# Performance work log

Hardware: AMD Instinct MI355X
Metric: run time of the kernel (lower is better)

The kernel has to match this reference:

```python
import jax, jax.numpy as jnp
import numpy as np

NUM_EMB = 1024
EMB_DIM = 256
COMM_COST = 0.25
BETA = 0.25


def setup_inputs() -> dict:
    key = jax.random.key(0)
    k1, k2 = jax.random.split(key)
    x = jax.random.normal(k1, (16, EMB_DIM, 64, 64), dtype=jnp.float32)
    # nn.Embedding initialized uniform(-1/num_emb, 1/num_emb)
    emb_weight = jax.random.uniform(
        k2, (NUM_EMB, EMB_DIM), dtype=jnp.float32,
        minval=-1.0 / NUM_EMB, maxval=1.0 / NUM_EMB)
    return {"x": x, "emb_weight": emb_weight}


def reference(x, emb_weight):
    # x: [B, C, H, W] -> [B, H, W, C]
    xp = jnp.transpose(x, (0, 2, 3, 1))
    B, H, W, C = xp.shape
    flat = xp.reshape(-1, C)  # [N, C]
    # squared euclidean distances (argmin-equivalent to torch.cdist)
    d2 = (jnp.sum(flat * flat, axis=1, keepdims=True)
          - 2.0 * jnp.einsum('nc,kc->nk', flat, emb_weight)
          + jnp.sum(emb_weight * emb_weight, axis=1))  # [N, K]
    idx = jnp.argmin(d2, axis=1)  # [N]
    quantized = emb_weight[idx].reshape(B, H, W, C)
    e_latent_loss = jnp.mean((jax.lax.stop_gradient(quantized) - xp) ** 2) * BETA
    q_latent_loss = jnp.mean((quantized - jax.lax.stop_gradient(xp)) ** 2)
    c_loss = q_latent_loss + COMM_COST * e_latent_loss
    # straight-through estimator
    quant_st = xp + jax.lax.stop_gradient(quantized - xp)
    quant_out = jnp.transpose(quant_st, (0, 3, 1, 2))  # [B, C, H, W]
    return (c_loss, quant_out)
```

## Files before the change

kernel.cpp:

```cpp
#include <hip/hip_runtime.h>
#include <hip/hip_bf16.h>
#include <cstdint>
#include <cstddef>

#define EMB_K   1024
#define EMB_C   256
#define HWB     4096
#define NPIX    65536

typedef __bf16 bf16x8 __attribute__((ext_vector_type(8)));
typedef float  f32x4  __attribute__((ext_vector_type(4)));

__device__ __forceinline__ unsigned short bf16bits(float v) {
  __hip_bfloat16 h = __float2bfloat16(v);
  return __builtin_bit_cast(unsigned short, h);
}

__global__ void k_emb(const float* __restrict__ emb, unsigned short* __restrict__ emb_bf,
                      float* __restrict__ enorm, float* __restrict__ loss,
                      unsigned* __restrict__ ctr) {
  int k = blockIdx.x;
  int c = threadIdx.x;
  if (k == 0 && c == 0) { *loss = 0.f; *ctr = 0u; }
  float v = emb[(size_t)k * EMB_C + c];
  emb_bf[(size_t)k * EMB_C + c] = bf16bits(v);
  float s = v * v;
  for (int m = 32; m; m >>= 1) s += __shfl_down(s, m, 64);
  __shared__ float red[4];
  int lane = c & 63, w = c >> 6;
  if (lane == 0) red[w] = s;
  __syncthreads();
  if (c == 0) enorm[k] = red[0] + red[1] + red[2] + red[3];
}

__device__ __forceinline__ void stage_b64(const unsigned short* __restrict__ embbf,
                                          unsigned char* buf, int kt, int t) {
#pragma unroll
  for (int j = 0; j < 4; ++j) {
    int d = j * 512 + t;
    int r = d >> 5;
    int slot = d & 31;
    int c16 = ((slot >> 3) << 3) | ((slot & 7) ^ (r & 7));
    const unsigned short* src = embbf + (size_t)(kt * 64 + r) * EMB_C + c16 * 8;
    __builtin_amdgcn_global_load_lds(
        (const __attribute__((address_space(1))) void*)src,
        (__attribute__((address_space(3))) void*)(buf + (unsigned)(j * 8192 + (t >> 6) * 1024)),
        16, 0, 0);
  }
}

#define LDS_BYTES 70688

__global__ __launch_bounds__(512, 4) void
k_main(const float* __restrict__ x, const float* __restrict__ emb,
       const unsigned short* __restrict__ embbf, const float* __restrict__ enorm,
       float* __restrict__ out, float* __restrict__ loss, unsigned* __restrict__ ctr) {
  extern __shared__ char smem[];
  unsigned char* R0 = (unsigned char*)smem;
  unsigned char* R1 = (unsigned char*)(smem + 32768);
  float*    cjl    = (float*)(smem + 65536);
  unsigned* keys_l = (unsigned*)(smem + 69632);
  float*    xn_l   = (float*)(smem + 70144);
  float*    red    = (float*)(smem + 70656);

  int n0  = blockIdx.x * 128;
  int b   = n0 >> 12;
  int hw0 = n0 & 4095;
  int t    = threadIdx.x;
  int w    = t >> 6, lane = t & 63;
  int quad = lane >> 4, lr = lane & 15;
  int g = w >> 1;
  int h = w & 1;

  for (int i = t; i < 1024; i += 512) cjl[i] = 0.375f - 0.5f * enorm[i];
  if (t < 128) { keys_l[t] = 0u; xn_l[t] = 0.f; }
  __syncthreads();

  {
    int nl = (w & 1) * 64 + lane;
    const float* xp = x + (size_t)b * (EMB_C * HWB) + hw0 + nl;
    float xn = 0.f;
#pragma unroll
    for (int o = 0; o < 8; ++o) {
      int cc = (w >> 1) * 8 + o;
      float v[8];
#pragma unroll
      for (int j = 0; j < 8; ++j) {
        v[j] = xp[(size_t)(cc * 8 + j) * HWB];
        xn += v[j] * v[j];
      }
      union { unsigned u[4]; uint4 q; } pk;
#pragma unroll
      for (int m = 0; m < 4; ++m)
        pk.u[m] = (unsigned)bf16bits(v[2 * m]) | ((unsigned)bf16bits(v[2 * m + 1]) << 16);
      int pos = ((cc >> 3) << 3) | ((cc & 7) ^ (nl & 7));
      *(uint4*)(R0 + nl * 512 + pos * 16) = pk.q;
    }
    atomicAdd(&xn_l[nl], xn);
  }
  __syncthreads();

  bf16x8 af[2][8];
#pragma unroll
  for (int i = 0; i < 2; ++i) {
    int rA = g * 32 + i * 16 + lr;
#pragma unroll
    for (int s = 0; s < 8; ++s) {
      int cc = s * 4 + quad;
      int pos = ((cc >> 3) << 3) | ((cc & 7) ^ (rA & 7));
      af[i][s] = *(const bf16x8*)(R0 + rA * 512 + pos * 16);
    }
  }
  __syncthreads();

  stage_b64(embbf, R0, 0, t);
  __syncthreads();

  unsigned best[2][4] = {{0u,0u,0u,0u},{0u,0u,0u,0u}};
  for (int kt = 0; kt < 16; ++kt) {
    unsigned char* srcB = (kt & 1) ? R1 : R0;
    unsigned char* dstB = (kt & 1) ? R0 : R1;
    if (kt < 15) stage_b64(embbf, dstB, kt + 1, t);
    float cj[2]; unsigned kp[2];
#pragma unroll
    for (int j = 0; j < 2; ++j) {
      int k = kt * 64 + h * 32 + j * 16 + lr;
      cj[j] = cjl[k];
      kp[j] = 1023u - (unsigned)k;
    }
    f32x4 acc[2][2] = {};
#pragma unroll
    for (int s = 0; s < 8; ++s) {
      bf16x8 bf[2];
#pragma unroll
      for (int j = 0; j < 2; ++j) {
        int rB = h * 32 + j * 16 + lr;
        int cc = s * 4 + quad;
        int pos = ((cc >> 3) << 3) | ((cc & 7) ^ (rB & 7));
        bf[j] = *(const bf16x8*)(srcB + rB * 512 + pos * 16);
      }
#pragma unroll
      for (int i = 0; i < 2; ++i)
#pragma unroll
        for (int j = 0; j < 2; ++j)
          acc[i][j] = __builtin_amdgcn_mfma_f32_16x16x32_bf16(af[i][s], bf[j], acc[i][j], 0, 0, 0);
    }
#pragma unroll
    for (int i = 0; i < 2; ++i)
#pragma unroll
      for (int j = 0; j < 2; ++j)
#pragma unroll
        for (int r = 0; r < 4; ++r) {
          float f = acc[i][j][r] + cj[j];
          unsigned key = (__float_as_uint(f) & 0xFFFFFC00u) | kp[j];
          best[i][r] = best[i][r] > key ? best[i][r] : key;
        }
    __syncthreads();
  }

#pragma unroll
  for (int i = 0; i < 2; ++i)
#pragma unroll
    for (int r = 0; r < 4; ++r) {
      unsigned v = best[i][r];
#pragma unroll
      for (int m = 1; m < 16; m <<= 1) {
        unsigned o = (unsigned)__shfl_xor((int)v, m, 64);
        v = v > o ? v : o;
      }
      if (lr == 0) atomicMax(&keys_l[g * 32 + i * 16 + quad * 4 + r], v);
    }
  __syncthreads();

  if (t < 128) {
    unsigned key = keys_l[t];
    float fh = __uint_as_float(key & 0xFFFFFC00u);
    float lsum = xn_l[t] + 0.75f - 2.0f * fh;
    for (int m = 32; m; m >>= 1) lsum += __shfl_down(lsum, m, 64);
    if (lane == 0) red[w] = lsum;
  }
  __syncthreads();
  if (t == 0) {
    atomicAdd(loss, red[0] + red[1]);
    __threadfence();
  }

  float* tile = (float*)R0;
  int nl  = t & 127;
  int cs  = (t >> 7) * 32;
  int idx = 1023 - (int)(keys_l[nl] & 1023u);
  float* ob = out + 1 + (size_t)b * (EMB_C * HWB) + hw0;
  for (int hc = 0; hc < 2; ++hc) {
    if (hc) __syncthreads();
    const float* er = emb + (size_t)idx * EMB_C + hc * 128 + cs;
#pragma unroll
    for (int m = 0; m < 8; ++m) {
      f32x4 q = *(const f32x4*)(er + m * 4);
      tile[(cs + m * 4 + 0) * 128 + nl] = q[0];
      tile[(cs + m * 4 + 1) * 128 + nl] = q[1];
      tile[(cs + m * 4 + 2) * 128 + nl] = q[2];
      tile[(cs + m * 4 + 3) * 128 + nl] = q[3];
    }
    __syncthreads();
#pragma unroll
    for (int s2 = 0; s2 < 32; ++s2) {
      int id = s2 * 512 + t;
      int cl = id >> 7;
      int nn = id & 127;
      ob[(size_t)(hc * 128 + cl) * HWB + nn] = tile[cl * 128 + nn];
    }
  }

  if (t == 0) {
    unsigned done = atomicAdd(ctr, 1u);
    if (done == gridDim.x - 1) {
      float total = atomicAdd(loss, 0.f);
      out[0] = 1.0625f * total / 16777216.0f;
    }
  }
}

extern "C" void kernel_launch(void* const* d_in, const int* in_sizes, int n_in,
                              void* d_out, int out_size, void* d_ws, size_t ws_size,
                              hipStream_t stream) {
  const float* x   = (const float*)d_in[0];
  const float* emb = (const float*)d_in[1];
  float* out = (float*)d_out;
  char*  ws  = (char*)d_ws;

  unsigned short* emb_bf = (unsigned short*)ws;
  float*          enorm  = (float*)(ws + 524288);
  float*          loss   = (float*)(ws + 528384);
  unsigned*       ctr    = (unsigned*)(ws + 528388);

  hipFuncSetAttribute((const void*)k_main,
                      hipFuncAttributeMaxDynamicSharedMemorySize, LDS_BYTES);

  k_emb <<<dim3(EMB_K), dim3(EMB_C), 0, stream>>>(emb, emb_bf, enorm, loss, ctr);
  k_main<<<dim3(NPIX / 128), dim3(512), LDS_BYTES, stream>>>(x, emb, emb_bf, enorm,
                                                             out, loss, ctr);
}
```

Measured before the change: 177.8 us.

## Split fused VQ kernel into transpose, GEMM-argmin, and gather-output kernels

Breaks the single fused kernel into three. The first transposes x and converts it to bf16 into a scratch area inside the output buffer, also producing per-pixel norms. The second is a GEMM with argmin whose warps now cover 64 rows by 16 codes each, with launch bounds lowered to 2 blocks. The third gathers codebook rows and writes the transposed output with vectorised stores. The aim is to separate memory-bound phases from the MFMA loop and make them more efficient, at the cost of extra launches and writing then re-reading the bf16 copy of x through global memory.

```diff
diff --git a/kernel.cpp b/kernel.cpp
--- a/kernel.cpp
+++ b/kernel.cpp
@@ -10,6 +10,7 @@
 
 typedef __bf16 bf16x8 __attribute__((ext_vector_type(8)));
 typedef float  f32x4  __attribute__((ext_vector_type(4)));
+typedef float  f32x4a __attribute__((ext_vector_type(4), aligned(4)));
 
 __device__ __forceinline__ unsigned short bf16bits(float v) {
   __hip_bfloat16 h = __float2bfloat16(v);
@@ -33,15 +34,57 @@
   if (c == 0) enorm[k] = red[0] + red[1] + red[2] + red[3];
 }
 
-__device__ __forceinline__ void stage_b64(const unsigned short* __restrict__ embbf,
-                                          unsigned char* buf, int kt, int t) {
+__global__ __launch_bounds__(256) void
+k_tr(const float* __restrict__ x, unsigned short* __restrict__ A,
+     float* __restrict__ xn_g) {
+  __shared__ unsigned char tile[64 * 512];
+  __shared__ float xn_l[64];
+  int t  = threadIdx.x;
+  int n0 = blockIdx.x * 64;
+  int b  = n0 >> 12, hw0 = n0 & 4095;
+  int nl = t & 63, qq = t >> 6;
+  if (t < 64) xn_l[t] = 0.f;
+  __syncthreads();
+  const float* xp = x + (size_t)b * (EMB_C * HWB) + hw0 + nl;
+  float xn = 0.f;
+#pragma unroll
+  for (int o = 0; o < 8; ++o) {
+    int cc = qq * 8 + o;
+    float v[8];
+#pragma unroll
+    for (int j = 0; j < 8; ++j) {
+      v[j] = xp[(size_t)(cc * 8 + j) * HWB];
+      xn += v[j] * v[j];
+    }
+    union { unsigned u[4]; uint4 q; } pk;
+#pragma unroll
+    for (int m = 0; m < 4; ++m)
+      pk.u[m] = (unsigned)bf16bits(v[2 * m]) | ((unsigned)bf16bits(v[2 * m + 1]) << 16);
+    int pos = ((cc >> 3) << 3) | ((cc & 7) ^ (nl & 7));
+    *(uint4*)(tile + nl * 512 + pos * 16) = pk.q;
+  }
+  atomicAdd(&xn_l[nl], xn);
+  __syncthreads();
+  if (t < 64) xn_g[n0 + t] = xn_l[t];
+  uint4* Adst = (uint4*)A + (size_t)n0 * 32;
+#pragma unroll
+  for (int k = 0; k < 8; ++k) {
+    int id = k * 256 + t;
+    int n = id >> 5, slot = id & 31;
+    int pos = ((slot >> 3) << 3) | ((slot & 7) ^ (n & 7));
+    Adst[id] = *(const uint4*)(tile + n * 512 + pos * 16);
+  }
+}
+
+__device__ __forceinline__ void stage64(const unsigned short* __restrict__ rows,
+                                        unsigned char* buf, int t) {
 #pragma unroll
   for (int j = 0; j < 4; ++j) {
     int d = j * 512 + t;
     int r = d >> 5;
     int slot = d & 31;
     int c16 = ((slot >> 3) << 3) | ((slot & 7) ^ (r & 7));
-    const unsigned short* src = embbf + (size_t)(kt * 64 + r) * EMB_C + c16 * 8;
+    const unsigned short* src = rows + (size_t)r * EMB_C + c16 * 8;
     __builtin_amdgcn_global_load_lds(
         (const __attribute__((address_space(1))) void*)src,
         (__attribute__((address_space(3))) void*)(buf + (unsigned)(j * 8192 + (t >> 6) * 1024)),
@@ -49,12 +92,13 @@
   }
 }
 
-#define LDS_BYTES 70688
-
-__global__ __launch_bounds__(512, 4) void
-k_main(const float* __restrict__ x, const float* __restrict__ emb,
-       const unsigned short* __restrict__ embbf, const float* __restrict__ enorm,
-       float* __restrict__ out, float* __restrict__ loss, unsigned* __restrict__ ctr) {
+#define K2_LDS 70688
+
+__global__ __launch_bounds__(512, 2) void
+k_gemm(const unsigned short* __restrict__ A, const unsigned short* __restrict__ embbf,
+       const float* __restrict__ enorm, const float* __restrict__ xn_g,
+       unsigned* __restrict__ keys_g, float* __restrict__ out,
+       float* __restrict__ loss, unsigned* __restrict__ ctr) {
   extern __shared__ char smem[];
   unsigned char* R0 = (unsigned char*)smem;
   unsigned char* R1 = (unsigned char*)(smem + 32768);
@@ -63,47 +107,22 @@
   float*    xn_l   = (float*)(smem + 70144);
   float*    red    = (float*)(smem + 70656);
 
-  int n0  = blockIdx.x * 128;
-  int b   = n0 >> 12;
-  int hw0 = n0 & 4095;
-  int t    = threadIdx.x;
-  int w    = t >> 6, lane = t & 63;
+  int n0 = blockIdx.x * 128;
+  int t = threadIdx.x, w = t >> 6, lane = t & 63;
   int quad = lane >> 4, lr = lane & 15;
-  int g = w >> 1;
-  int h = w & 1;
-
+  int g  = w >> 2;
+  int h2 = w & 3;
+
+  stage64(A + (size_t)n0 * EMB_C, R0, t);
+  stage64(A + (size_t)(n0 + 64) * EMB_C, R1, t);
   for (int i = t; i < 1024; i += 512) cjl[i] = 0.375f - 0.5f * enorm[i];
-  if (t < 128) { keys_l[t] = 0u; xn_l[t] = 0.f; }
-  __syncthreads();
-
-  {
-    int nl = (w & 1) * 64 + lane;
-    const float* xp = x + (size_t)b * (EMB_C * HWB) + hw0 + nl;
-    float xn = 0.f;
-#pragma unroll
-    for (int o = 0; o < 8; ++o) {
-      int cc = (w >> 1) * 8 + o;
-      float v[8];
-#pragma unroll
-      for (int j = 0; j < 8; ++j) {
-        v[j] = xp[(size_t)(cc * 8 + j) * HWB];
-        xn += v[j] * v[j];
-      }
-      union { unsigned u[4]; uint4 q; } pk;
-#pragma unroll
-      for (int m = 0; m < 4; ++m)
-        pk.u[m] = (unsigned)bf16bits(v[2 * m]) | ((unsigned)bf16bits(v[2 * m + 1]) << 16);
-      int pos = ((cc >> 3) << 3) | ((cc & 7) ^ (nl & 7));
-      *(uint4*)(R0 + nl * 512 + pos * 16) = pk.q;
-    }
-    atomicAdd(&xn_l[nl], xn);
-  }
-  __syncthreads();
-
-  bf16x8 af[2][8];
-#pragma unroll
-  for (int i = 0; i < 2; ++i) {
-    int rA = g * 32 + i * 16 + lr;
+  if (t < 128) { keys_l[t] = 0u; xn_l[t] = xn_g[n0 + t]; }
+  __syncthreads();
+
+  bf16x8 af[4][8];
+#pragma unroll
+  for (int i = 0; i < 4; ++i) {
+    int rA = g * 64 + i * 16 + lr;
 #pragma unroll
     for (int s = 0; s < 8; ++s) {
       int cc = s * 4 + quad;
@@ -113,53 +132,40 @@
   }
   __syncthreads();
 
-  stage_b64(embbf, R0, 0, t);
-  __syncthreads();
-
-  unsigned best[2][4] = {{0u,0u,0u,0u},{0u,0u,0u,0u}};
+  stage64(embbf, R0, t);
+  __syncthreads();
+
+  unsigned best[4][4] = {};
   for (int kt = 0; kt < 16; ++kt) {
     unsigned char* srcB = (kt & 1) ? R1 : R0;
     unsigned char* dstB = (kt & 1) ? R0 : R1;
-    if (kt < 15) stage_b64(embbf, dstB, kt + 1, t);
-    float cj[2]; unsigned kp[2];
-#pragma unroll
-    for (int j = 0; j < 2; ++j) {
-      int k = kt * 64 + h * 32 + j * 16 + lr;
-      cj[j] = cjl[k];
-      kp[j] = 1023u - (unsigned)k;
-    }
-    f32x4 acc[2][2] = {};
+    if (kt < 15) stage64(embbf + (size_t)(kt + 1) * 64 * EMB_C, dstB, t);
+    float cj; unsigned kp;
+    { int k = kt * 64 + h2 * 16 + lr; cj = cjl[k]; kp = 1023u - (unsigned)k; }
+    f32x4 acc[4] = {};
 #pragma unroll
     for (int s = 0; s < 8; ++s) {
-      bf16x8 bf[2];
-#pragma unroll
-      for (int j = 0; j < 2; ++j) {
-        int rB = h * 32 + j * 16 + lr;
-        int cc = s * 4 + quad;
-        int pos = ((cc >> 3) << 3) | ((cc & 7) ^ (rB & 7));
-        bf[j] = *(const bf16x8*)(srcB + rB * 512 + pos * 16);
+      int cc = s * 4 + quad;
+      int rB = h2 * 16 + lr;
+      int pos = ((cc >> 3) << 3) | ((cc & 7) ^ (rB & 7));
+      bf16x8 bf = *(const bf16x8*)(srcB + rB * 512 + pos * 16);
+#pragma unroll
+      for (int i = 0; i < 4; ++i)
+        acc[i] = __builtin_amdgcn_mfma_f32_16x16x32_bf16(af[i][s], bf, acc[i], 0, 0, 0);
+    }
+#pragma unroll
+    for (int i = 0; i < 4; ++i)
+#pragma unroll
+      for (int r = 0; r < 4; ++r) {
+        float f = acc[i][r] + cj;
+        unsigned key = (__float_as_uint(f) & 0xFFFFFC00u) | kp;
+        best[i][r] = best[i][r] > key ? best[i][r] : key;
       }
-#pragma unroll
-      for (int i = 0; i < 2; ++i)
-#pragma unroll
-        for (int j = 0; j < 2; ++j)
-          acc[i][j] = __builtin_amdgcn_mfma_f32_16x16x32_bf16(af[i][s], bf[j], acc[i][j], 0, 0, 0);
-    }
-#pragma unroll
-    for (int i = 0; i < 2; ++i)
-#pragma unroll
-      for (int j = 0; j < 2; ++j)
-#pragma unroll
-        for (int r = 0; r < 4; ++r) {
-          float f = acc[i][j][r] + cj[j];
-          unsigned key = (__float_as_uint(f) & 0xFFFFFC00u) | kp[j];
-          best[i][r] = best[i][r] > key ? best[i][r] : key;
-        }
     __syncthreads();
   }
 
 #pragma unroll
-  for (int i = 0; i < 2; ++i)
+  for (int i = 0; i < 4; ++i)
 #pragma unroll
     for (int r = 0; r < 4; ++r) {
       unsigned v = best[i][r];
@@ -168,12 +174,13 @@
         unsigned o = (unsigned)__shfl_xor((int)v, m, 64);
         v = v > o ? v : o;
       }
-      if (lr == 0) atomicMax(&keys_l[g * 32 + i * 16 + quad * 4 + r], v);
+      if (lr == 0) atomicMax(&keys_l[g * 64 + i * 16 + quad * 4 + r], v);
     }
   __syncthreads();
 
   if (t < 128) {
     unsigned key = keys_l[t];
+    keys_g[n0 + t] = key;
     float fh = __uint_as_float(key & 0xFFFFFC00u);
     float lsum = xn_l[t] + 0.75f - 2.0f * fh;
     for (int m = 32; m; m >>= 1) lsum += __shfl_down(lsum, m, 64);
@@ -183,39 +190,42 @@
   if (t == 0) {
     atomicAdd(loss, red[0] + red[1]);
     __threadfence();
-  }
-
-  float* tile = (float*)R0;
-  int nl  = t & 127;
-  int cs  = (t >> 7) * 32;
-  int idx = 1023 - (int)(keys_l[nl] & 1023u);
-  float* ob = out + 1 + (size_t)b * (EMB_C * HWB) + hw0;
-  for (int hc = 0; hc < 2; ++hc) {
-    if (hc) __syncthreads();
-    const float* er = emb + (size_t)idx * EMB_C + hc * 128 + cs;
-#pragma unroll
-    for (int m = 0; m < 8; ++m) {
-      f32x4 q = *(const f32x4*)(er + m * 4);
-      tile[(cs + m * 4 + 0) * 128 + nl] = q[0];
-      tile[(cs + m * 4 + 1) * 128 + nl] = q[1];
-      tile[(cs + m * 4 + 2) * 128 + nl] = q[2];
-      tile[(cs + m * 4 + 3) * 128 + nl] = q[3];
-    }
-    __syncthreads();
-#pragma unroll
-    for (int s2 = 0; s2 < 32; ++s2) {
-      int id = s2 * 512 + t;
-      int cl = id >> 7;
-      int nn = id & 127;
-      ob[(size_t)(hc * 128 + cl) * HWB + nn] = tile[cl * 128 + nn];
-    }
-  }
-
-  if (t == 0) {
     unsigned done = atomicAdd(ctr, 1u);
     if (done == gridDim.x - 1) {
       float total = atomicAdd(loss, 0.f);
       out[0] = 1.0625f * total / 16777216.0f;
+    }
+  }
+}
+
+__global__ __launch_bounds__(512) void
+k_out(const float* __restrict__ emb, const unsigned* __restrict__ keys_g,
+      float* __restrict__ out) {
+  extern __shared__ float tile[];
+  int t  = threadIdx.x;
+  int n0 = blockIdx.x * 256;
+  int b  = n0 >> 12, hw0 = n0 & 4095;
+  int w  = t >> 6, lane = t & 63;
+  int n  = t >> 1, ch = t & 1;
+  int idx = 1023 - (int)(keys_g[n0 + n] & 1023u);
+  const float* er = emb + (size_t)idx * EMB_C;
+  float* ob = out + 1 + (size_t)b * (EMB_C * HWB) + hw0;
+  for (int p = 0; p < 4; ++p) {
+    int c0 = p * 64;
+    if (p) __syncthreads();
+#pragma unroll
+    for (int jj = 0; jj < 8; ++jj) {
+      f32x4 q = *(const f32x4*)(er + c0 + ch * 32 + jj * 4);
+#pragma unroll
+      for (int m = 0; m < 4; ++m)
+        tile[(ch * 32 + jj * 4 + m) * 256 + n] = q[m];
+    }
+    __syncthreads();
+#pragma unroll
+    for (int cc = 0; cc < 8; ++cc) {
+      int cl = w * 8 + cc;
+      f32x4 q = *(const f32x4*)(tile + cl * 256 + lane * 4);
+      *(f32x4a*)(ob + (size_t)(c0 + cl) * HWB + lane * 4) = q;
     }
   }
 }
@@ -232,11 +242,19 @@
   float*          enorm  = (float*)(ws + 524288);
   float*          loss   = (float*)(ws + 528384);
   unsigned*       ctr    = (unsigned*)(ws + 528388);
-
-  hipFuncSetAttribute((const void*)k_main,
-                      hipFuncAttributeMaxDynamicSharedMemorySize, LDS_BYTES);
-
-  k_emb <<<dim3(EMB_K), dim3(EMB_C), 0, stream>>>(emb, emb_bf, enorm, loss, ctr);
-  k_main<<<dim3(NPIX / 128), dim3(512), LDS_BYTES, stream>>>(x, emb, emb_bf, enorm,
-                                                             out, loss, ctr);
-}
+  float*          xn_g   = (float*)(ws + 532480);
+  unsigned*       keys_g = (unsigned*)(ws + 794624);
+
+  unsigned short* A = (unsigned short*)(out + 4);
+
+  hipFuncSetAttribute((const void*)k_gemm,
+                      hipFuncAttributeMaxDynamicSharedMemorySize, K2_LDS);
+  hipFuncSetAttribute((const void*)k_out,
+                      hipFuncAttributeMaxDynamicSharedMemorySize, 65536);
+
+  k_emb <<<dim3(EMB_K),      dim3(EMB_C), 0,      stream>>>(emb, emb_bf, enorm, loss, ctr);
+  k_tr  <<<dim3(NPIX / 64),  dim3(256),   0,      stream>>>(x, A, xn_g);
+  k_gemm<<<dim3(NPIX / 128), dim3(512),   K2_LDS, stream>>>(A, emb_bf, enorm, xn_g,
+                                                            keys_g, out, loss, ctr);
+  k_out <<<dim3(NPIX / 256), dim3(512),   65536,  stream>>>(emb, keys_g, out);
+}
```

Result: slower. 187.1 us (+5.2%).

## Double pixel tile to 256 per 1024-thread block with vectorized x loads and stores

Applied to the files above, without the earlier changes.

Each block now covers 256 pixels with 1024 threads, so every staged 64-row codebook tile is reused by twice as many pixels and the total codebook traffic through LDS is halved. The x tile is loaded with float4 reads and packed to bf16 in two passes, and the output write uses a rotated LDS tile so that unaligned output (offset by one float for the loss slot) can be written with float4 stores. In exchange, blocks are larger with fewer resident per CU, and the grid is halved, which may reduce latency hiding and load balance.

```diff
diff --git a/kernel.cpp b/kernel.cpp
--- a/kernel.cpp
+++ b/kernel.cpp
@@ -33,118 +33,120 @@
   if (c == 0) enorm[k] = red[0] + red[1] + red[2] + red[3];
 }
 
-__device__ __forceinline__ void stage_b64(const unsigned short* __restrict__ embbf,
-                                          unsigned char* buf, int kt, int t) {
-#pragma unroll
-  for (int j = 0; j < 4; ++j) {
-    int d = j * 512 + t;
+__device__ __forceinline__ void stage64b(const unsigned short* __restrict__ rows,
+                                         unsigned char* buf, int t) {
+#pragma unroll
+  for (int j = 0; j < 2; ++j) {
+    int d = j * 1024 + t;
     int r = d >> 5;
     int slot = d & 31;
     int c16 = ((slot >> 3) << 3) | ((slot & 7) ^ (r & 7));
-    const unsigned short* src = embbf + (size_t)(kt * 64 + r) * EMB_C + c16 * 8;
+    const unsigned short* src = rows + (size_t)r * EMB_C + c16 * 8;
     __builtin_amdgcn_global_load_lds(
         (const __attribute__((address_space(1))) void*)src,
-        (__attribute__((address_space(3))) void*)(buf + (unsigned)(j * 8192 + (t >> 6) * 1024)),
+        (__attribute__((address_space(3))) void*)(buf + (unsigned)(j * 16384 + (t >> 6) * 1024)),
         16, 0, 0);
   }
 }
 
-#define LDS_BYTES 70688
-
-__global__ __launch_bounds__(512, 4) void
+#define LDS_BYTES 71744
+
+__global__ __launch_bounds__(1024) void
 k_main(const float* __restrict__ x, const float* __restrict__ emb,
        const unsigned short* __restrict__ embbf, const float* __restrict__ enorm,
        float* __restrict__ out, float* __restrict__ loss, unsigned* __restrict__ ctr) {
   extern __shared__ char smem[];
-  unsigned char* R0 = (unsigned char*)smem;
-  unsigned char* R1 = (unsigned char*)(smem + 32768);
   float*    cjl    = (float*)(smem + 65536);
   unsigned* keys_l = (unsigned*)(smem + 69632);
-  float*    xn_l   = (float*)(smem + 70144);
-  float*    red    = (float*)(smem + 70656);
-
-  int n0  = blockIdx.x * 128;
-  int b   = n0 >> 12;
-  int hw0 = n0 & 4095;
-  int t    = threadIdx.x;
-  int w    = t >> 6, lane = t & 63;
+  float*    xn_l   = (float*)(smem + 70656);
+  float*    red    = (float*)(smem + 71680);
+
+  int n0 = blockIdx.x * 256;
+  int b  = n0 >> 12, hw0 = n0 & 4095;
+  int t = threadIdx.x, w = t >> 6, lane = t & 63;
   int quad = lane >> 4, lr = lane & 15;
-  int g = w >> 1;
-  int h = w & 1;
-
-  for (int i = t; i < 1024; i += 512) cjl[i] = 0.375f - 0.5f * enorm[i];
-  if (t < 128) { keys_l[t] = 0u; xn_l[t] = 0.f; }
-  __syncthreads();
-
-  {
-    int nl = (w & 1) * 64 + lane;
-    const float* xp = x + (size_t)b * (EMB_C * HWB) + hw0 + nl;
-    float xn = 0.f;
-#pragma unroll
-    for (int o = 0; o < 8; ++o) {
-      int cc = (w >> 1) * 8 + o;
-      float v[8];
+  int g  = w >> 1;
+  int h2 = w & 1;
+
+  if (t < 256) { keys_l[t] = 0u; xn_l[t] = 0.f; }
+  for (int i = t; i < 1024; i += 1024) cjl[i] = 0.375f - 0.5f * enorm[i];
+  __syncthreads();
+
+  bf16x8 af[2][8];
+#pragma unroll
+  for (int p = 0; p < 2; ++p) {
+    if (p) __syncthreads();
+    {
+      int hwq = t & 31;
+      int cg  = t >> 5;
+      const float* xp = x + (size_t)b * (EMB_C * HWB) + hw0 + p * 128 + hwq * 4;
+      float xn[4] = {0.f, 0.f, 0.f, 0.f};
+      unsigned pk[4][4] = {};
 #pragma unroll
       for (int j = 0; j < 8; ++j) {
-        v[j] = xp[(size_t)(cc * 8 + j) * HWB];
-        xn += v[j] * v[j];
-      }
-      union { unsigned u[4]; uint4 q; } pk;
-#pragma unroll
-      for (int m = 0; m < 4; ++m)
-        pk.u[m] = (unsigned)bf16bits(v[2 * m]) | ((unsigned)bf16bits(v[2 * m + 1]) << 16);
-      int pos = ((cc >> 3) << 3) | ((cc & 7) ^ (nl & 7));
-      *(uint4*)(R0 + nl * 512 + pos * 16) = pk.q;
-    }
-    atomicAdd(&xn_l[nl], xn);
-  }
-  __syncthreads();
-
-  bf16x8 af[2][8];
-#pragma unroll
-  for (int i = 0; i < 2; ++i) {
-    int rA = g * 32 + i * 16 + lr;
+        f32x4 v = *(const f32x4*)(xp + (size_t)(cg * 8 + j) * HWB);
+#pragma unroll
+        for (int m = 0; m < 4; ++m) {
+          xn[m] += v[m] * v[m];
+          pk[m][j >> 1] |= (unsigned)bf16bits(v[m]) << ((j & 1) * 16);
+        }
+      }
+#pragma unroll
+      for (int m = 0; m < 4; ++m) {
+        int nl = hwq * 4 + m;
+        int pos = ((cg >> 3) << 3) | ((cg & 7) ^ (nl & 7));
+        *(uint4*)(smem + nl * 512 + pos * 16) = *(const uint4*)pk[m];
+        atomicAdd(&xn_l[p * 128 + nl], xn[m]);
+      }
+    }
+    __syncthreads();
+    if ((g >> 2) == p) {
+#pragma unroll
+      for (int i = 0; i < 2; ++i) {
+        int rA = (g & 3) * 32 + i * 16 + lr;
+#pragma unroll
+        for (int s = 0; s < 8; ++s) {
+          int cc = s * 4 + quad;
+          int pos = ((cc >> 3) << 3) | ((cc & 7) ^ (rA & 7));
+          af[i][s] = *(const bf16x8*)(smem + rA * 512 + pos * 16);
+        }
+      }
+    }
+  }
+  __syncthreads();
+
+  stage64b(embbf, (unsigned char*)smem, t);
+  __syncthreads();
+
+  unsigned best[2][4] = {};
+  int posB = 0;
+  for (int kt = 0; kt < 16; ++kt) {
+    unsigned char* srcB = (unsigned char*)smem + ((kt & 1) << 15);
+    unsigned char* dstB = (unsigned char*)smem + (((kt + 1) & 1) << 15);
+    if (kt < 15) stage64b(embbf + (size_t)(kt + 1) * 64 * EMB_C, dstB, t);
+    float cj[2]; unsigned kp[2];
+#pragma unroll
+    for (int j = 0; j < 2; ++j) {
+      int k = kt * 64 + h2 * 32 + j * 16 + lr;
+      cj[j] = cjl[k];
+      kp[j] = 1023u - (unsigned)k;
+    }
+    f32x4 acc[2][2] = {};
 #pragma unroll
     for (int s = 0; s < 8; ++s) {
       int cc = s * 4 + quad;
-      int pos = ((cc >> 3) << 3) | ((cc & 7) ^ (rA & 7));
-      af[i][s] = *(const bf16x8*)(R0 + rA * 512 + pos * 16);
-    }
-  }
-  __syncthreads();
-
-  stage_b64(embbf, R0, 0, t);
-  __syncthreads();
-
-  unsigned best[2][4] = {{0u,0u,0u,0u},{0u,0u,0u,0u}};
-  for (int kt = 0; kt < 16; ++kt) {
-    unsigned char* srcB = (kt & 1) ? R1 : R0;
-    unsigned char* dstB = (kt & 1) ? R0 : R1;
-    if (kt < 15) stage_b64(embbf, dstB, kt + 1, t);
-    float cj[2]; unsigned kp[2];
-#pragma unroll
-    for (int j = 0; j < 2; ++j) {
-      int k = kt * 64 + h * 32 + j * 16 + lr;
-      cj[j] = cjl[k];
-      kp[j] = 1023u - (unsigned)k;
-    }
-    f32x4 acc[2][2] = {};
-#pragma unroll
-    for (int s = 0; s < 8; ++s) {
+      int pos = ((cc >> 3) << 3) | ((cc & 7) ^ (lr & 7));
       bf16x8 bf[2];
 #pragma unroll
-      for (int j = 0; j < 2; ++j) {
-        int rB = h * 32 + j * 16 + lr;
-        int cc = s * 4 + quad;
-        int pos = ((cc >> 3) << 3) | ((cc & 7) ^ (rB & 7));
-        bf[j] = *(const bf16x8*)(srcB + rB * 512 + pos * 16);
-      }
+      for (int j = 0; j < 2; ++j)
+        bf[j] = *(const bf16x8*)(srcB + (h2 * 32 + j * 16 + lr) * 512 + pos * 16);
 #pragma unroll
       for (int i = 0; i < 2; ++i)
 #pragma unroll
         for (int j = 0; j < 2; ++j)
           acc[i][j] = __builtin_amdgcn_mfma_f32_16x16x32_bf16(af[i][s], bf[j], acc[i][j], 0, 0, 0);
     }
+    (void)posB;
 #pragma unroll
     for (int i = 0; i < 2; ++i)
 #pragma unroll
@@ -172,7 +174,7 @@
     }
   __syncthreads();
 
-  if (t < 128) {
+  if (t < 256) {
     unsigned key = keys_l[t];
     float fh = __uint_as_float(key & 0xFFFFFC00u);
     float lsum = xn_l[t] + 0.75f - 2.0f * fh;
@@ -181,33 +183,38 @@
   }
   __syncthreads();
   if (t == 0) {
-    atomicAdd(loss, red[0] + red[1]);
+    atomicAdd(loss, red[0] + red[1] + red[2] + red[3]);
     __threadfence();
   }
 
-  float* tile = (float*)R0;
-  int nl  = t & 127;
-  int cs  = (t >> 7) * 32;
-  int idx = 1023 - (int)(keys_l[nl] & 1023u);
+  float* tile = (float*)smem;
+  int nn = t >> 2, ch = t & 3;
+  int idx = 1023 - (int)(keys_l[nn] & 1023u);
+  const float* er = emb + (size_t)idx * EMB_C;
+  int nrot = (nn - 3) & 255;
   float* ob = out + 1 + (size_t)b * (EMB_C * HWB) + hw0;
-  for (int hc = 0; hc < 2; ++hc) {
-    if (hc) __syncthreads();
-    const float* er = emb + (size_t)idx * EMB_C + hc * 128 + cs;
-#pragma unroll
-    for (int m = 0; m < 8; ++m) {
-      f32x4 q = *(const f32x4*)(er + m * 4);
-      tile[(cs + m * 4 + 0) * 128 + nl] = q[0];
-      tile[(cs + m * 4 + 1) * 128 + nl] = q[1];
-      tile[(cs + m * 4 + 2) * 128 + nl] = q[2];
-      tile[(cs + m * 4 + 3) * 128 + nl] = q[3];
+  for (int p = 0; p < 4; ++p) {
+    int c0 = p * 64;
+    if (p) __syncthreads();
+#pragma unroll
+    for (int q = 0; q < 4; ++q) {
+      f32x4 v = *(const f32x4*)(er + c0 + ch * 16 + q * 4);
+#pragma unroll
+      for (int m = 0; m < 4; ++m)
+        tile[(ch * 16 + q * 4 + m) * 256 + nrot] = v[m];
     }
     __syncthreads();
 #pragma unroll
-    for (int s2 = 0; s2 < 32; ++s2) {
-      int id = s2 * 512 + t;
-      int cl = id >> 7;
-      int nn = id & 127;
-      ob[(size_t)(hc * 128 + cl) * HWB + nn] = tile[cl * 128 + nn];
+    for (int cc = 0; cc < 4; ++cc) {
+      int cl = w * 4 + cc;
+      const float* tr = tile + cl * 256;
+      float* F = ob + (size_t)(c0 + cl) * HWB;
+      if (lane < 63) {
+        f32x4 q = *(const f32x4*)(tr + 4 * lane);
+        *(f32x4*)(F + 3 + 4 * lane) = q;
+      }
+      if (lane == 0) { F[0] = tr[253]; F[1] = tr[254]; F[2] = tr[255]; }
+      if (lane == 63) { F[255] = tr[252]; }
     }
   }
 
@@ -236,7 +243,7 @@
   hipFuncSetAttribute((const void*)k_main,
                       hipFuncAttributeMaxDynamicSharedMemorySize, LDS_BYTES);
 
-  k_emb <<<dim3(EMB_K), dim3(EMB_C), 0, stream>>>(emb, emb_bf, enorm, loss, ctr);
-  k_main<<<dim3(NPIX / 128), dim3(512), LDS_BYTES, stream>>>(x, emb, emb_bf, enorm,
-                                                             out, loss, ctr);
-}
+  k_emb <<<dim3(EMB_K),      dim3(EMB_C), 0,         stream>>>(emb, emb_bf, enorm, loss, ctr);
+  k_main<<<dim3(NPIX / 256), dim3(1024),  LDS_BYTES, stream>>>(x, emb, emb_bf, enorm,
+                                                               out, loss, ctr);
+}
```

New measurement: 159.9 us. -10.1%, faster.
